# Kernel tuning notes

Hardware: AMD Instinct MI355X
Metric: run time of the kernel (lower is better)

The kernel has to match this reference:

```python
import jax, jax.numpy as jnp
import numpy as np

B, S, D, H = 4, 2048, 1024, 16
DK = D // H


def setup_inputs() -> dict:
    key = jax.random.key(0)
    ks = jax.random.split(key, 8)
    scale = 1.0 / np.sqrt(D)
    return {
        "q": jax.random.normal(ks[0], (B, S, D), jnp.float32),
        "k": jax.random.normal(ks[1], (B, S, D), jnp.float32),
        "v": jax.random.normal(ks[2], (B, S, D), jnp.float32),
        "mask": jnp.ones((1,), jnp.int32),  # unused (original code never applies it)
        "W_Q": jax.random.normal(ks[3], (D, D), jnp.float32) * scale,
        "W_K": jax.random.normal(ks[4], (D, D), jnp.float32) * scale,
        "W_V": jax.random.normal(ks[5], (D, D), jnp.float32) * scale,
        "W_O": jax.random.normal(ks[6], (D, D), jnp.float32) * scale,
    }


def reference(q, k, v, mask, W_Q, W_K, W_V, W_O):
    # nn.Linear(bias=False): y = x @ W.T ; weight shape [out, in]
    query = q @ W_Q.T  # [B,S,D]
    key_ = k @ W_K.T
    value = v @ W_V.T
    # split heads -> [B,H,S,DK]
    query = query.reshape(B, S, H, DK).transpose(0, 2, 1, 3)
    key_ = key_.reshape(B, S, H, DK).transpose(0, 2, 1, 3)
    value = value.reshape(B, S, H, DK).transpose(0, 2, 1, 3)
    # naive attention: full [B,H,S,S] score matrix (faithful to source)
    scores = jnp.einsum("bhqd,bhkd->bhqk", query, key_) / jnp.sqrt(
        jnp.asarray(DK, query.dtype)
    )
    attn = jax.nn.softmax(scores, axis=-1)  # dropout p=0.0 -> identity
    x = jnp.einsum("bhqk,bhkd->bhqd", attn, value)  # [B,H,S,DK]
    x = x.transpose(0, 2, 1, 3).reshape(B, S, D)
    return x @ W_O.T
```

## Files before the change

### kernel.cpp

```cpp
#include <hip/hip_runtime.h>
#include <math.h>


#define DEV __device__ __forceinline__

typedef __bf16 bf16x8 __attribute__((ext_vector_type(8)));
typedef __bf16 bf16x2 __attribute__((ext_vector_type(2)));
typedef float f32x4 __attribute__((ext_vector_type(4)));
typedef unsigned int u32x2 __attribute__((ext_vector_type(2)));

typedef __attribute__((address_space(1))) const unsigned int g_u32;
typedef __attribute__((address_space(3))) unsigned int l_u32;

DEV unsigned short f2bf(float x) {
  unsigned int u = __float_as_uint(x);
  u += 0x7fffu + ((u >> 16) & 1u);
  return (unsigned short)(u >> 16);
}

DEV unsigned int pack2bf(float a, float b) {
#if __has_builtin(__builtin_amdgcn_cvt_pk_bf16_f32)
  bf16x2 r = __builtin_amdgcn_cvt_pk_bf16_f32(a, b);
  union { bf16x2 v; unsigned int u; } c;
  c.v = r;
  return c.u;
#else
  unsigned int ua = __float_as_uint(a) + 0x8000u;
  unsigned int ub = __float_as_uint(b) + 0x8000u;
  return (ua >> 16) | (ub & 0xffff0000u);
#endif
}

DEV float fexp2(float x) {
#if __has_builtin(__builtin_amdgcn_exp2f)
  return __builtin_amdgcn_exp2f(x);
#else
  return __expf(x * 0.69314718056f);
#endif
}

DEV void ld16(const unsigned short* g, unsigned short* l) {
  __builtin_amdgcn_global_load_lds((g_u32*)g, (l_u32*)l, 16, 0, 0);
}

__global__ __launch_bounds__(256) void cast_all(
    const float* __restrict__ q, const float* __restrict__ k,
    const float* __restrict__ v, const float* __restrict__ w0,
    const float* __restrict__ w1, const float* __restrict__ w2,
    const float* __restrict__ w3, unsigned short* __restrict__ qb,
    unsigned short* __restrict__ kb, unsigned short* __restrict__ vb,
    unsigned short* __restrict__ o0, unsigned short* __restrict__ o1,
    unsigned short* __restrict__ o2, unsigned short* __restrict__ o3) {
  const int bb = blockIdx.x;
  const float* src;
  unsigned short* dst;
  int i;
  if (bb < 24576) {
    const int z = bb >> 13, lb = bb & 8191;
    src = (z == 0) ? q : (z == 1) ? k : v;
    dst = (z == 0) ? qb : (z == 1) ? kb : vb;
    i = lb * 256 + threadIdx.x;
  } else {
    const int t = bb - 24576;
    const int z = t >> 10, lb = t & 1023;
    src = (z == 0) ? w0 : (z == 1) ? w1 : (z == 2) ? w2 : w3;
    dst = (z == 0) ? o0 : (z == 1) ? o1 : (z == 2) ? o2 : o3;
    i = lb * 256 + threadIdx.x;
  }
  float4 vv = reinterpret_cast<const float4*>(src)[i];
  ushort4 o;
  o.x = f2bf(vv.x); o.y = f2bf(vv.y); o.z = f2bf(vv.z); o.w = f2bf(vv.w);
  reinterpret_cast<ushort4*>(dst)[i] = o;
}

template <bool SW>
DEV void gemm_core(const unsigned short* __restrict__ A,
                   const unsigned short* __restrict__ W,
                   unsigned short* As, unsigned short* Bs,
                   f32x4 (&acc)[4][4], int tileM, int tileN) {
  const int tid = threadIdx.x;
  const int w = tid >> 6, lane = tid & 63;
  const int wr = (w & 1) * 64, wc = (w >> 1) * 64;
  const int l15 = lane & 15, g4 = lane >> 4, l7 = l15 & 7;
  const int rsub = lane >> 3;
  const int gsrc = (lane & 7) ^ rsub;

  const f32x4 fzero = {0.f, 0.f, 0.f, 0.f};
#pragma unroll
  for (int i = 0; i < 4; i++)
#pragma unroll
    for (int j = 0; j < 4; j++) acc[i][j] = fzero;

  for (int k0 = 0; k0 < 1024; k0 += 64) {
#pragma unroll
    for (int j = 0; j < 4; ++j) {
      const int c = w * 4 + j;
      ld16(A + (size_t)(tileM + c * 8 + rsub) * 1024 + k0 + gsrc * 8, As + c * 512);
      ld16(W + (size_t)(tileN + c * 8 + rsub) * 1024 + k0 + gsrc * 8, Bs + c * 512);
    }
    __syncthreads();
#pragma unroll
    for (int kc = 0; kc < 2; kc++) {
      const int ph = ((kc * 4 + g4) ^ l7) * 8;
      bf16x8 aF[4], bF[4];
#pragma unroll
      for (int i = 0; i < 4; i++)
        aF[i] = *reinterpret_cast<const bf16x8*>(&As[(wr + i * 16 + l15) * 64 + ph]);
#pragma unroll
      for (int j = 0; j < 4; j++)
        bF[j] = *reinterpret_cast<const bf16x8*>(&Bs[(wc + j * 16 + l15) * 64 + ph]);
#pragma unroll
      for (int i = 0; i < 4; i++)
#pragma unroll
        for (int j = 0; j < 4; j++) {
          if (SW)
            acc[j][i] = __builtin_amdgcn_mfma_f32_16x16x32_bf16(bF[j], aF[i], acc[j][i], 0, 0, 0);
          else
            acc[i][j] = __builtin_amdgcn_mfma_f32_16x16x32_bf16(aF[i], bF[j], acc[i][j], 0, 0, 0);
        }
    }
    __syncthreads();
  }
}

__global__ __launch_bounds__(256) void gemm_qkv(
    const unsigned short* __restrict__ qb, const unsigned short* __restrict__ kb,
    const unsigned short* __restrict__ vb, const unsigned short* __restrict__ Wq,
    const unsigned short* __restrict__ Wk, const unsigned short* __restrict__ Wv,
    unsigned short* __restrict__ Qp, unsigned short* __restrict__ Kp,
    unsigned short* __restrict__ VpT) {
  __shared__ __align__(16) unsigned short As[128 * 64];
  __shared__ __align__(16) unsigned short Bs[128 * 64];
  const int z = blockIdx.z;
  const int tileM = blockIdx.x * 128, tileN = blockIdx.y * 128;
  const int tid = threadIdx.x, w = tid >> 6, lane = tid & 63;
  const int wr = (w & 1) * 64, wc = (w >> 1) * 64;
  const int l15 = lane & 15, g4 = lane >> 4;
  f32x4 acc[4][4];

  if (z < 2) {
    gemm_core<true>((z == 0) ? qb : kb, (z == 0) ? Wq : Wk, As, Bs, acc, tileM, tileN);
    const float qs = (z == 0) ? 0.125f * 1.44269504089f : 1.0f;
    unsigned short* C = (z == 0) ? Qp : Kp;
#pragma unroll
    for (int i = 0; i < 4; i++) {
      const size_t row = (size_t)(tileM + wr + i * 16 + l15);
#pragma unroll
      for (int j = 0; j < 4; j++) {
        const int col = tileN + wc + j * 16 + g4 * 4;
        ushort4 pk;
        pk.x = f2bf(acc[j][i][0] * qs); pk.y = f2bf(acc[j][i][1] * qs);
        pk.z = f2bf(acc[j][i][2] * qs); pk.w = f2bf(acc[j][i][3] * qs);
        *reinterpret_cast<ushort4*>(&C[row * 1024 + col]) = pk;
      }
    }
  } else {
    gemm_core<false>(vb, Wv, As, Bs, acc, tileM, tileN);
    const int b = tileM / 2048, s0 = tileM % 2048;
#pragma unroll
    for (int i = 0; i < 4; i++)
#pragma unroll
      for (int j = 0; j < 4; j++) {
        int col = tileN + wc + j * 16 + l15;
        int s = s0 + wr + i * 16 + g4 * 4;
        ushort4 pk;
        pk.x = f2bf(acc[i][j][0]); pk.y = f2bf(acc[i][j][1]);
        pk.z = f2bf(acc[i][j][2]); pk.w = f2bf(acc[i][j][3]);
        *reinterpret_cast<ushort4*>(&VpT[(size_t)(b * 1024 + col) * 2048 + s]) = pk;
      }
  }
}

__global__ __launch_bounds__(256) void gemm_out(
    const unsigned short* __restrict__ Xp, const unsigned short* __restrict__ Wo,
    float* __restrict__ out) {
  __shared__ __align__(16) unsigned short As[128 * 64];
  __shared__ __align__(16) unsigned short Bs[128 * 64];
  const int tileM = blockIdx.x * 128, tileN = blockIdx.y * 128;
  f32x4 acc[4][4];
  gemm_core<true>(Xp, Wo, As, Bs, acc, tileM, tileN);
  const int tid = threadIdx.x, w = tid >> 6, lane = tid & 63;
  const int wr = (w & 1) * 64, wc = (w >> 1) * 64;
  const int l15 = lane & 15, g4 = lane >> 4;
#pragma unroll
  for (int i = 0; i < 4; i++) {
    const size_t row = (size_t)(tileM + wr + i * 16 + l15);
#pragma unroll
    for (int j = 0; j < 4; j++) {
      const int col = tileN + wc + j * 16 + g4 * 4;
      *reinterpret_cast<f32x4*>(&out[row * 1024 + col]) = acc[j][i];
    }
  }
}

__global__ __launch_bounds__(256, 2) void attn(
    const unsigned short* __restrict__ Qp, const unsigned short* __restrict__ Kp,
    const unsigned short* __restrict__ VpT, unsigned short* __restrict__ Xp) {
  __shared__ __align__(16) unsigned short Ks[2 * 64 * 64];
  __shared__ __align__(16) unsigned short Vs[2 * 64 * 64];
  __shared__ __align__(16) unsigned short Ps[4 * 4 * 1024];

  const int bid = blockIdx.x;
  const int nid = (bid & 7) * 64 + (bid >> 3);
  const int qt = nid & 7, bh = nid >> 3;
  const int b = bh >> 4, h = bh & 15;
  const int q0 = qt * 256;
  const int tid = threadIdx.x, w = tid >> 6, lane = tid & 63;
  const int l15 = lane & 15, g4 = lane >> 4;
  const int l7 = l15 & 7;

  const int rsub = lane >> 3;
  const int gsrc = (lane & 7) ^ rsub;

  bf16x8 qf[4][2];
#pragma unroll
  for (int mi = 0; mi < 4; mi++) {
    const unsigned short* Qrow =
        Qp + (size_t)(b * 2048 + q0 + w * 64 + mi * 16 + l15) * 1024 + h * 64;
    qf[mi][0] = *reinterpret_cast<const bf16x8*>(Qrow + g4 * 8);
    qf[mi][1] = *reinterpret_cast<const bf16x8*>(Qrow + 32 + g4 * 8);
  }

  const f32x4 fzero = {0.f, 0.f, 0.f, 0.f};
  f32x4 o[4][4];
#pragma unroll
  for (int mi = 0; mi < 4; mi++)
#pragma unroll
    for (int dj = 0; dj < 4; dj++) o[mi][dj] = fzero;
  float l_i[4] = {0.f, 0.f, 0.f, 0.f};

  const unsigned short* Kbase = Kp + (size_t)(b * 2048) * 1024 + h * 64;
  const unsigned short* Vbase = VpT + (size_t)(b * 1024 + h * 64) * 2048;
  unsigned short* Pw = Ps + w * 4096;

  const int c = w * 2;

#pragma unroll
  for (int j = 0; j < 2; ++j) {
    ld16(Kbase + (size_t)((c + j) * 8 + rsub) * 1024 + gsrc * 8, Ks + (c + j) * 512);
    ld16(Vbase + (size_t)((c + j) * 8 + rsub) * 2048 + gsrc * 8, Vs + (c + j) * 512);
  }
  __syncthreads();

  int cur = 0;
  for (int t = 0; t < 32; ++t) {
    const int kt = t * 64;
    unsigned short* Kc = Ks + cur * 4096;
    unsigned short* Vc = Vs + cur * 4096;

    if (t < 31) {
      unsigned short* Kn = Ks + (cur ^ 1) * 4096;
      unsigned short* Vn = Vs + (cur ^ 1) * 4096;
      const int ktn = kt + 64;
#pragma unroll
      for (int j = 0; j < 2; ++j) {
        ld16(Kbase + (size_t)(ktn + (c + j) * 8 + rsub) * 1024 + gsrc * 8,
             Kn + (c + j) * 512);
        ld16(Vbase + (size_t)((c + j) * 8 + rsub) * 2048 + ktn + gsrc * 8,
             Vn + (c + j) * 512);
      }
    }

    f32x4 sv[4][4];
    __builtin_amdgcn_s_setprio(1);
#pragma unroll
    for (int jt = 0; jt < 4; jt++) {
      const int row = jt * 16 + l15;
      const int s0 = g4 ^ l7;
      bf16x8 kf0 = *reinterpret_cast<const bf16x8*>(&Kc[row * 64 + s0 * 8]);
      bf16x8 kf1 = *reinterpret_cast<const bf16x8*>(&Kc[row * 64 + (s0 ^ 4) * 8]);
#pragma unroll
      for (int mi = 0; mi < 4; mi++) {
        f32x4 z = fzero;
        z = __builtin_amdgcn_mfma_f32_16x16x32_bf16(kf0, qf[mi][0], z, 0, 0, 0);
        z = __builtin_amdgcn_mfma_f32_16x16x32_bf16(kf1, qf[mi][1], z, 0, 0, 0);
        sv[mi][jt] = z;
      }
    }
    __builtin_amdgcn_s_setprio(0);

#pragma unroll
    for (int mi = 0; mi < 4; mi++) {
      float rs = 0.f;
#pragma unroll
      for (int jt = 0; jt < 4; jt++)
#pragma unroll
        for (int r = 0; r < 4; r++) {
          sv[mi][jt][r] = fexp2(sv[mi][jt][r]);
          rs += sv[mi][jt][r];
        }
      l_i[mi] += rs;
#pragma unroll
      for (int jt = 0; jt < 4; jt++) {
        u32x2 pk;
        pk.x = pack2bf(sv[mi][jt][0], sv[mi][jt][1]);
        pk.y = pack2bf(sv[mi][jt][2], sv[mi][jt][3]);
        const int slot = (jt * 4 + g4) ^ l15;
        *reinterpret_cast<u32x2*>(&Pw[mi * 1024 + l15 * 64 + slot * 4]) = pk;
      }
    }

    bf16x8 vf[2][4];
#pragma unroll
    for (int kc = 0; kc < 2; kc++)
#pragma unroll
      for (int dj = 0; dj < 4; dj++)
        vf[kc][dj] = *reinterpret_cast<const bf16x8*>(
            &Vc[(dj * 16 + l15) * 64 + ((kc * 4 + g4) ^ l7) * 8]);

    __builtin_amdgcn_s_setprio(1);
#pragma unroll
    for (int mi = 0; mi < 4; mi++) {
#pragma unroll
      for (int kc = 0; kc < 2; kc++) {
        const int sA = (kc * 8 + g4 * 2) ^ l15;
        const int sB = (kc * 8 + g4 * 2 + 1) ^ l15;
        u32x2 pa = *reinterpret_cast<const u32x2*>(&Pw[mi * 1024 + l15 * 64 + sA * 4]);
        u32x2 pb = *reinterpret_cast<const u32x2*>(&Pw[mi * 1024 + l15 * 64 + sB * 4]);
        union { unsigned int u[4]; bf16x8 v; } pf;
        pf.u[0] = pa.x; pf.u[1] = pa.y; pf.u[2] = pb.x; pf.u[3] = pb.y;
#pragma unroll
        for (int dj = 0; dj < 4; dj++)
          o[mi][dj] = __builtin_amdgcn_mfma_f32_16x16x32_bf16(vf[kc][dj], pf.v,
                                                             o[mi][dj], 0, 0, 0);
      }
    }
    __builtin_amdgcn_s_setprio(0);

    __syncthreads();
    cur ^= 1;
  }

#pragma unroll
  for (int mi = 0; mi < 4; mi++) {
    float rs = l_i[mi];
    rs += __shfl_xor(rs, 16);
    rs += __shfl_xor(rs, 32);
    const float inv = 1.f / rs;
    const size_t row = (size_t)(b * 2048 + q0 + w * 64 + mi * 16 + l15);
#pragma unroll
    for (int dj = 0; dj < 4; dj++) {
      ushort4 pk;
      pk.x = f2bf(o[mi][dj][0] * inv);
      pk.y = f2bf(o[mi][dj][1] * inv);
      pk.z = f2bf(o[mi][dj][2] * inv);
      pk.w = f2bf(o[mi][dj][3] * inv);
      *reinterpret_cast<ushort4*>(&Xp[row * 1024 + h * 64 + dj * 16 + g4 * 4]) = pk;
    }
  }
}

extern "C" void kernel_launch(void* const* d_in, const int* in_sizes, int n_in,
                              void* d_out, int out_size, void* d_ws, size_t ws_size,
                              hipStream_t stream) {
  const float* q  = (const float*)d_in[0];
  const float* k  = (const float*)d_in[1];
  const float* v  = (const float*)d_in[2];
  const float* Wq = (const float*)d_in[4];
  const float* Wk = (const float*)d_in[5];
  const float* Wv = (const float*)d_in[6];
  const float* Wo = (const float*)d_in[7];
  float* out = (float*)d_out;

  char* ws = (char*)d_ws;
  const size_t MB = 1u << 20;
  unsigned short* qb  = (unsigned short*)(ws + 0 * MB);
  unsigned short* kb  = (unsigned short*)(ws + 16 * MB);
  unsigned short* vb  = (unsigned short*)(ws + 32 * MB);
  unsigned short* wqb = (unsigned short*)(ws + 48 * MB);
  unsigned short* wkb = (unsigned short*)(ws + 50 * MB);
  unsigned short* wvb = (unsigned short*)(ws + 52 * MB);
  unsigned short* wob = (unsigned short*)(ws + 54 * MB);
  unsigned short* Qp  = (unsigned short*)(ws + 56 * MB);
  unsigned short* Kp  = (unsigned short*)(ws + 72 * MB);
  unsigned short* VpT = (unsigned short*)(ws + 88 * MB);
  unsigned short* Xp  = (unsigned short*)(ws + 104 * MB);

  cast_all<<<dim3(28672), 256, 0, stream>>>(q, k, v, Wq, Wk, Wv, Wo,
                                            qb, kb, vb, wqb, wkb, wvb, wob);

  dim3 gq(64, 8, 3);
  gemm_qkv<<<gq, 256, 0, stream>>>(qb, kb, vb, wqb, wkb, wvb, Qp, Kp, VpT);

  attn<<<dim3(512), 256, 0, stream>>>(Qp, Kp, VpT, Xp);

  dim3 go(64, 8, 1);
  gemm_out<<<go, 256, 0, stream>>>(Xp, wob, out);
}
```

Before: 355.4 us.

## Interleave softmax exp with PV MFMAs using a single-tile P buffer per wave

```diff
diff --git a/kernel.cpp b/kernel.cpp
--- a/kernel.cpp
+++ b/kernel.cpp
@@ -193,12 +193,12 @@
   }
 }
 
-__global__ __launch_bounds__(256, 2) void attn(
+__global__ __launch_bounds__(256, 4) void attn(
     const unsigned short* __restrict__ Qp, const unsigned short* __restrict__ Kp,
     const unsigned short* __restrict__ VpT, unsigned short* __restrict__ Xp) {
   __shared__ __align__(16) unsigned short Ks[2 * 64 * 64];
   __shared__ __align__(16) unsigned short Vs[2 * 64 * 64];
-  __shared__ __align__(16) unsigned short Ps[4 * 4 * 1024];
+  __shared__ __align__(16) unsigned short Ps[4 * 1024];
 
   const int bid = blockIdx.x;
   const int nid = (bid & 7) * 64 + (bid >> 3);
@@ -231,7 +231,7 @@
 
   const unsigned short* Kbase = Kp + (size_t)(b * 2048) * 1024 + h * 64;
   const unsigned short* Vbase = VpT + (size_t)(b * 1024 + h * 64) * 2048;
-  unsigned short* Pw = Ps + w * 4096;
+  unsigned short* Pw = Ps + w * 1024;
 
   const int c = w * 2;
 
@@ -279,27 +279,6 @@
     }
     __builtin_amdgcn_s_setprio(0);
 
-#pragma unroll
-    for (int mi = 0; mi < 4; mi++) {
-      float rs = 0.f;
-#pragma unroll
-      for (int jt = 0; jt < 4; jt++)
-#pragma unroll
-        for (int r = 0; r < 4; r++) {
-          sv[mi][jt][r] = fexp2(sv[mi][jt][r]);
-          rs += sv[mi][jt][r];
-        }
-      l_i[mi] += rs;
-#pragma unroll
-      for (int jt = 0; jt < 4; jt++) {
-        u32x2 pk;
-        pk.x = pack2bf(sv[mi][jt][0], sv[mi][jt][1]);
-        pk.y = pack2bf(sv[mi][jt][2], sv[mi][jt][3]);
-        const int slot = (jt * 4 + g4) ^ l15;
-        *reinterpret_cast<u32x2*>(&Pw[mi * 1024 + l15 * 64 + slot * 4]) = pk;
-      }
-    }
-
     bf16x8 vf[2][4];
 #pragma unroll
     for (int kc = 0; kc < 2; kc++)
@@ -308,24 +287,70 @@
         vf[kc][dj] = *reinterpret_cast<const bf16x8*>(
             &Vc[(dj * 16 + l15) * 64 + ((kc * 4 + g4) ^ l7) * 8]);
 
-    __builtin_amdgcn_s_setprio(1);
+    {
+      float rs = 0.f;
+#pragma unroll
+      for (int jt = 0; jt < 4; jt++)
+#pragma unroll
+        for (int r = 0; r < 4; r++) {
+          sv[0][jt][r] = fexp2(sv[0][jt][r]);
+          rs += sv[0][jt][r];
+        }
+      l_i[0] += rs;
+#pragma unroll
+      for (int jt = 0; jt < 4; jt++) {
+        u32x2 pk;
+        pk.x = pack2bf(sv[0][jt][0], sv[0][jt][1]);
+        pk.y = pack2bf(sv[0][jt][2], sv[0][jt][3]);
+        const int slot = (jt * 4 + g4) ^ l15;
+        *reinterpret_cast<u32x2*>(&Pw[l15 * 64 + slot * 4]) = pk;
+      }
+    }
+
 #pragma unroll
     for (int mi = 0; mi < 4; mi++) {
+      u32x2 pa[2], pb[2];
 #pragma unroll
       for (int kc = 0; kc < 2; kc++) {
         const int sA = (kc * 8 + g4 * 2) ^ l15;
         const int sB = (kc * 8 + g4 * 2 + 1) ^ l15;
-        u32x2 pa = *reinterpret_cast<const u32x2*>(&Pw[mi * 1024 + l15 * 64 + sA * 4]);
-        u32x2 pb = *reinterpret_cast<const u32x2*>(&Pw[mi * 1024 + l15 * 64 + sB * 4]);
+        pa[kc] = *reinterpret_cast<const u32x2*>(&Pw[l15 * 64 + sA * 4]);
+        pb[kc] = *reinterpret_cast<const u32x2*>(&Pw[l15 * 64 + sB * 4]);
+      }
+
+      if (mi < 3) {
+        float rs = 0.f;
+#pragma unroll
+        for (int jt = 0; jt < 4; jt++)
+#pragma unroll
+          for (int r = 0; r < 4; r++) {
+            sv[mi + 1][jt][r] = fexp2(sv[mi + 1][jt][r]);
+            rs += sv[mi + 1][jt][r];
+          }
+        l_i[mi + 1] += rs;
+#pragma unroll
+        for (int jt = 0; jt < 4; jt++) {
+          u32x2 pk;
+          pk.x = pack2bf(sv[mi + 1][jt][0], sv[mi + 1][jt][1]);
+          pk.y = pack2bf(sv[mi + 1][jt][2], sv[mi + 1][jt][3]);
+          const int slot = (jt * 4 + g4) ^ l15;
+          *reinterpret_cast<u32x2*>(&Pw[l15 * 64 + slot * 4]) = pk;
+        }
+      }
+
+      __builtin_amdgcn_s_setprio(1);
+#pragma unroll
+      for (int kc = 0; kc < 2; kc++) {
         union { unsigned int u[4]; bf16x8 v; } pf;
-        pf.u[0] = pa.x; pf.u[1] = pa.y; pf.u[2] = pb.x; pf.u[3] = pb.y;
+        pf.u[0] = pa[kc].x; pf.u[1] = pa[kc].y;
+        pf.u[2] = pb[kc].x; pf.u[3] = pb[kc].y;
 #pragma unroll
         for (int dj = 0; dj < 4; dj++)
           o[mi][dj] = __builtin_amdgcn_mfma_f32_16x16x32_bf16(vf[kc][dj], pf.v,
                                                              o[mi][dj], 0, 0, 0);
       }
-    }
-    __builtin_amdgcn_s_setprio(0);
+      __builtin_amdgcn_s_setprio(0);
+    }
 
     __syncthreads();
     cur ^= 1;
```

New measurement: 747.7 us. 2.1x slower.
